# Kernel tuning notes

Measured on AMD Instinct MI355X. Metric: run time of the kernel, lower is better.

Reference implementation:

```python
import jax, jax.numpy as jnp
import numpy as np

B, T, D, R, V = 32, 14, 1024, 4, 8192


def setup_inputs() -> dict:
    key = jax.random.key(0)
    k1, k2, k3, k4, k5 = jax.random.split(key, 5)
    input_embs = jax.random.normal(k1, (B, T, D), dtype=jnp.float32)
    label_ids = jax.random.randint(k2, (B, T), 0, V)
    w_alpha = jax.random.normal(k3, (D, R), dtype=jnp.float32)
    w_beta = jax.random.normal(k4, (D, R), dtype=jnp.float32)
    w_vocab = jax.random.normal(k5, (D, V * R * R), dtype=jnp.float32)
    return {"input_embs": input_embs, "label_ids": label_ids,
            "w_alpha": w_alpha, "w_beta": w_beta, "w_vocab": w_vocab}


def _tt_params(x, w_alpha, w_beta, w_vocab):
    b, t, d = x.shape
    r = w_alpha.shape[1]
    v = w_vocab.shape[1] // (r * r)
    xf = x.reshape(-1, d)
    alpha = jax.nn.sigmoid((xf @ w_alpha).reshape(b, t, r).mean(1)) + 0.001   # (B,R)
    beta = jax.nn.sigmoid((xf @ w_beta).reshape(b, t, r).mean(1)) + 0.001     # (B,R)
    core = jax.nn.sigmoid((xf @ w_vocab).reshape(b, t, r, v, r).mean(1)) * 0.01 + 0.001  # (B,R,V,R)
    return alpha, beta, core


def _chain_matmul(init, mats):
    # init: (B,R,R); mats: (n,B,R,R) -> sequential product init @ mats[0] @ ...
    def step(carry, m):
        return jnp.einsum('bik,bkj->bij', carry, m), None
    out, _ = jax.lax.scan(step, init, mats)
    return out


def reference(input_embs, label_ids, w_alpha, w_beta, w_vocab):
    alpha, beta, core = _tt_params(input_embs, w_alpha, w_beta, w_vocab)
    b, t = label_ids.shape
    # ---- _select: gather core slices at label indices, chain-multiply ----
    sel = core[jnp.arange(b)[:, None], :, label_ids, :]   # (B,T,R,R)
    sel = jnp.swapaxes(sel, 0, 1)                         # (T,B,R,R)
    chain = _chain_matmul(sel[0], sel[1:])                # (B,R,R)
    unnorm = jnp.einsum('bi,bij,bj->b', alpha, chain, beta)
    # ---- normalization: marginalized core multiplied T extra times (T+1 factors, as in source) ----
    cm = core.sum(axis=2)                                 # (B,R,R)
    cm_rep = jnp.broadcast_to(cm, (t,) + cm.shape)        # (T,B,R,R)
    nres = _chain_matmul(cm, cm_rep)                      # (B,R,R)
    norm = jnp.einsum('bi,bij,bj->b', alpha, nres, beta)
    probs = unnorm / norm + 0.001
    loss = -jnp.log(probs)
    return loss.mean()
```

## Files before the change

kernel.cpp:

```cpp
#include <hip/hip_runtime.h>
#include <cstdint>
#include <cstddef>

#define BB 32
#define TT 14
#define DD 1024
#define RR 4
#define VV 8192
#define NCOL (VV*RR*RR)

typedef float f32x16 __attribute__((ext_vector_type(16)));
typedef float f4 __attribute__((ext_vector_type(4)));
typedef short short8 __attribute__((ext_vector_type(8)));
typedef unsigned int uint;


__device__ __forceinline__ uint pack2(float a, float b) {
    return __builtin_amdgcn_perm(__builtin_bit_cast(uint, b),
                                 __builtin_bit_cast(uint, a), 0x07060302u);
}

__device__ __forceinline__ short8 packw(const float* w) {
    uint4 u = make_uint4(pack2(w[0], w[1]), pack2(w[2], w[3]),
                         pack2(w[4], w[5]), pack2(w[6], w[7]));
    return __builtin_bit_cast(short8, u);
}

__global__ __launch_bounds__(256) void k_prep_all(const float* __restrict__ in,
                                                  const float* __restrict__ wa,
                                                  const float* __restrict__ wb,
                                                  ushort* __restrict__ xfrag_us,
                                                  float* __restrict__ alpha,
                                                  float* __restrict__ beta,
                                                  float* __restrict__ cm) {
    __shared__ float xl[DD];
    const int b   = blockIdx.x;
    const int tid = threadIdx.x;
    const int d0  = tid * 4;

    f4 s4 = (f4){0.f, 0.f, 0.f, 0.f};
    #pragma unroll
    for (int t = 0; t < TT; ++t) {
        f4 v = *reinterpret_cast<const f4*>(&in[((b * TT + t) << 10) + d0]);
        s4 += v;
    }
    s4 *= (1.0f / TT);
    *reinterpret_cast<f4*>(&xl[d0]) = s4;

    if (b == 0) { cm[tid] = 0.f; cm[tid + 256] = 0.f; }

    {
        const int s  = d0 >> 4;
        const int h  = (d0 >> 3) & 1;
        const int j0 = d0 & 7;
        uint2 u;
        u.x = pack2(s4.x, s4.y);
        u.y = pack2(s4.z, s4.w);
        *reinterpret_cast<uint2*>(&xfrag_us[((s * 64 + b + 32 * h) << 3) + j0]) = u;
    }

    __syncthreads();

    const int wave = tid >> 6, lane = tid & 63;
    for (int p = wave; p < 8; p += 4) {
        const int r = p >> 1, sf = p & 1;
        const float* wm = sf ? wb : wa;
        float acc = 0.f;
        #pragma unroll
        for (int k = 0; k < 16; ++k) {
            int d = lane + 64 * k;
            acc += xl[d] * wm[d * RR + r];
        }
        #pragma unroll
        for (int m = 1; m < 64; m <<= 1) acc += __shfl_xor(acc, m);
        if (lane == 0) {
            float v = 1.0f / (1.0f + __expf(-acc)) + 0.001f;
            (sf ? beta : alpha)[b * RR + r] = v;
        }
    }
}

#define LOADW(DST, STEP)                                                      \
    _Pragma("unroll")                                                         \
    for (int j = 0; j < 8; ++j)                                               \
        DST[j] = __builtin_nontemporal_load(                                  \
            wp + (size_t)((STEP) * 16 + j) * NCOL);

#define MFMA_STEP(AX, WBUF)                                                   \
    acc = __builtin_amdgcn_mfma_f32_32x32x16_bf16(                            \
        __builtin_bit_cast(short8, AX), packw(WBUF), acc, 0, 0, 0);

__global__ __launch_bounds__(256, 4) void k_core(const float* __restrict__ wv,
                                                 const uint4* __restrict__ xfrag,
                                                 const int*   __restrict__ lab,
                                                 float* __restrict__ cm,
                                                 float* __restrict__ sel) {
    const int tid  = threadIdx.x;
    const int lane = tid & 63;
    const int wvid = tid >> 6;
    const int n0   = blockIdx.x * 128 + wvid * 32;
    const int n    = n0 + (lane & 31);
    const int ii   = n >> 15;
    const int jj   = n & 3;
    const int vv   = (n >> 2) & (VV - 1);

    __shared__ int   lds_lab[BB * TT];
    __shared__ float cm_blk[BB][4];

    const float* wp = wv + (size_t)((lane >> 5) * 8) * NCOL + n;

    f32x16 acc;
    #pragma unroll
    for (int q = 0; q < 16; ++q) acc[q] = 0.f;

    float w0[8], w1[8], w2[8], w3[8];
    uint4 ax0, ax1, ax2, ax3;
    LOADW(w0, 0); ax0 = xfrag[lane];
    LOADW(w1, 1); ax1 = xfrag[64 + lane];
    LOADW(w2, 2); ax2 = xfrag[128 + lane];
    LOADW(w3, 3); ax3 = xfrag[192 + lane];

    #pragma unroll 1
    for (int s = 0; s < 60; s += 4) {
        MFMA_STEP(ax0, w0); LOADW(w0, s + 4); ax0 = xfrag[((s + 4) << 6) + lane];
        MFMA_STEP(ax1, w1); LOADW(w1, s + 5); ax1 = xfrag[((s + 5) << 6) + lane];
        MFMA_STEP(ax2, w2); LOADW(w2, s + 6); ax2 = xfrag[((s + 6) << 6) + lane];
        MFMA_STEP(ax3, w3); LOADW(w3, s + 7); ax3 = xfrag[((s + 7) << 6) + lane];
    }
    MFMA_STEP(ax0, w0);
    MFMA_STEP(ax1, w1);
    MFMA_STEP(ax2, w2);
    MFMA_STEP(ax3, w3);

    for (int idx = tid; idx < BB * TT; idx += 256) lds_lab[idx] = lab[idx];
    if (tid < BB * 4) ((float*)cm_blk)[tid] = 0.f;
    __syncthreads();

    #pragma unroll
    for (int r = 0; r < 16; ++r) {
        float c = 0.01f / (1.0f + __expf(-acc[r])) + 0.001f;
        const int b = (r & 3) + 8 * (r >> 2) + 4 * (lane >> 5);
        float sred = c;
        sred += __shfl_xor(sred, 4);
        sred += __shfl_xor(sred, 8);
        sred += __shfl_xor(sred, 16);
        if ((lane & 31) < 4) atomicAdd(&cm_blk[b][lane & 3], sred);
        #pragma unroll
        for (int t = 0; t < TT; ++t)
            if (lds_lab[b * TT + t] == vv)
                sel[(b * TT + t) * 16 + (ii << 2) + jj] = c;
    }
    __syncthreads();
    if (tid < BB * 4) {
        int b = tid >> 2, j = tid & 3;
        atomicAdd(&cm[b * 16 + (ii << 2) + j], ((float*)cm_blk)[tid]);
    }
}

__global__ __launch_bounds__(64) void k_final(const float* __restrict__ cm,
                                              const float* __restrict__ sel,
                                              const float* __restrict__ alpha,
                                              const float* __restrict__ beta,
                                              float* __restrict__ out) {
    __shared__ float ls[BB];
    int b = threadIdx.x;
    if (b < BB) {
        float ch[16], tmp[16];
        #pragma unroll
        for (int q = 0; q < 16; ++q) ch[q] = sel[(b * TT + 0) * 16 + q];
        for (int t = 1; t < TT; ++t) {
            const float* m = &sel[(b * TT + t) * 16];
            #pragma unroll
            for (int i2 = 0; i2 < 4; ++i2)
                #pragma unroll
                for (int j2 = 0; j2 < 4; ++j2) {
                    float s = 0.f;
                    #pragma unroll
                    for (int k = 0; k < 4; ++k) s += ch[i2*4+k] * m[k*4+j2];
                    tmp[i2*4+j2] = s;
                }
            #pragma unroll
            for (int q = 0; q < 16; ++q) ch[q] = tmp[q];
        }

        float M[16], P[16];
        #pragma unroll
        for (int q = 0; q < 16; ++q) { M[q] = cm[b*16+q]; P[q] = M[q]; }
        for (int t = 0; t < TT; ++t) {
            #pragma unroll
            for (int i2 = 0; i2 < 4; ++i2)
                #pragma unroll
                for (int j2 = 0; j2 < 4; ++j2) {
                    float s = 0.f;
                    #pragma unroll
                    for (int k = 0; k < 4; ++k) s += P[i2*4+k] * M[k*4+j2];
                    tmp[i2*4+j2] = s;
                }
            #pragma unroll
            for (int q = 0; q < 16; ++q) P[q] = tmp[q];
        }

        float a[4], be[4];
        #pragma unroll
        for (int r = 0; r < 4; ++r) { a[r] = alpha[b*4+r]; be[r] = beta[b*4+r]; }
        float un = 0.f, no = 0.f;
        #pragma unroll
        for (int i2 = 0; i2 < 4; ++i2)
            #pragma unroll
            for (int j2 = 0; j2 < 4; ++j2) {
                un += a[i2] * ch[i2*4+j2] * be[j2];
                no += a[i2] * P [i2*4+j2] * be[j2];
            }
        float prob = un / no + 0.001f;
        ls[b] = -logf(prob);
    }
    __syncthreads();
    if (threadIdx.x == 0) {
        float s = 0.f;
        for (int q = 0; q < BB; ++q) s += ls[q];
        out[0] = s / BB;
    }
}

extern "C" void kernel_launch(void* const* d_in, const int* in_sizes, int n_in,
                              void* d_out, int out_size, void* d_ws, size_t ws_size,
                              hipStream_t stream) {
    const float* in_embs = (const float*)d_in[0];
    const int*   lab     = (const int*)  d_in[1];
    const float* wa      = (const float*)d_in[2];
    const float* wb      = (const float*)d_in[3];
    const float* wv      = (const float*)d_in[4];

    float* ws    = (float*)d_ws;
    float* cm    = ws;
    float* sel   = ws + 512;
    float* alpha = ws + 7680;
    float* beta  = ws + 7808;
    uint4* xfrag = (uint4*)(ws + 7936);

    k_prep_all<<<32,   256, 0, stream>>>(in_embs, wa, wb, (ushort*)xfrag,
                                         alpha, beta, cm);
    k_core    <<<1024, 256, 0, stream>>>(wv, xfrag, lab, cm, sel);
    k_final   <<<1,    64,  0, stream>>>(cm, sel, alpha, beta, (float*)d_out);
}
```

Measured before the change: 120.3 us.

## Stage weight tiles into LDS via async global_load_lds with multi-buffer pipeline

The core GEMV-like kernel now copies weight tiles from global memory straight into a four-slot LDS ring using global_load_lds, with explicit vmcnt waits and barriers. Each wave then reads its 8-row fragments from LDS and issues two MFMAs per stage. The block grows to 512 threads covering 512 columns, so the grid shrinks from 1024 to 256 blocks. The goal is fully coalesced, deeper-in-flight loads of the 2 GB/s-bound weight stream, traded against barrier overhead, 128KB of LDS per block, and lower block count and occupancy.

```diff
diff --git a/kernel.cpp b/kernel.cpp
--- a/kernel.cpp
+++ b/kernel.cpp
@@ -8,6 +8,8 @@
 #define RR 4
 #define VV 8192
 #define NCOL (VV*RR*RR)
+#define COLS 512
+#define NTHR 512
 
 typedef float f32x16 __attribute__((ext_vector_type(16)));
 typedef float f4 __attribute__((ext_vector_type(4)));
@@ -80,81 +82,117 @@
     }
 }
 
-#define LOADW(DST, STEP)                                                      \
-    _Pragma("unroll")                                                         \
-    for (int j = 0; j < 8; ++j)                                               \
-        DST[j] = __builtin_nontemporal_load(                                  \
-            wp + (size_t)((STEP) * 16 + j) * NCOL);
-
-#define MFMA_STEP(AX, WBUF)                                                   \
-    acc = __builtin_amdgcn_mfma_f32_32x32x16_bf16(                            \
-        __builtin_bit_cast(short8, AX), packw(WBUF), acc, 0, 0, 0);
-
-__global__ __launch_bounds__(256, 4) void k_core(const float* __restrict__ wv,
+#define STAGE(SG, AXREG)                                                      \
+    do {                                                                      \
+        const int bi_ = (SG) & 3;                                             \
+        _Pragma("unroll")                                                     \
+        for (int r_ = 0; r_ < 4; ++r_) {                                      \
+            const float* gp_ = wv + (size_t)(16 * (SG) + 4 * r_ + srow) * NCOL\
+                               + n0 + scol;                                   \
+            __builtin_amdgcn_global_load_lds(                                 \
+                (const __attribute__((address_space(1))) void*)gp_,           \
+                (__attribute__((address_space(3))) void*)                     \
+                    &buf[bi_][4 * r_ + srow][scol],                           \
+                16, 0, 0);                                                    \
+        }                                                                     \
+        AXREG = xf[((SG) << 6) + lane];                                       \
+    } while (0)
+
+#define COMPUTE(SG, AXREG)                                                    \
+    do {                                                                      \
+        const int bi_ = (SG) & 3;                                             \
+        _Pragma("unroll")                                                     \
+        for (int tau_ = 0; tau_ < 2; ++tau_) {                                \
+            float wr_[8];                                                     \
+            _Pragma("unroll")                                                 \
+            for (int j_ = 0; j_ < 8; ++j_)                                    \
+                wr_[j_] = buf[bi_][rbase + j_][cloc + tau_ * 32];             \
+            acc[tau_] = __builtin_amdgcn_mfma_f32_32x32x16_bf16(              \
+                __builtin_bit_cast(short8, AXREG), packw(wr_), acc[tau_],     \
+                0, 0, 0);                                                     \
+        }                                                                     \
+    } while (0)
+
+#define VMWAIT(N) asm volatile("s_waitcnt vmcnt(" #N ")" ::: "memory")
+#define BAR()     __builtin_amdgcn_s_barrier()
+
+__global__ __launch_bounds__(512, 2) void k_core(const float* __restrict__ wv,
                                                  const uint4* __restrict__ xfrag,
                                                  const int*   __restrict__ lab,
                                                  float* __restrict__ cm,
                                                  float* __restrict__ sel) {
     const int tid  = threadIdx.x;
     const int lane = tid & 63;
-    const int wvid = tid >> 6;
-    const int n0   = blockIdx.x * 128 + wvid * 32;
-    const int n    = n0 + (lane & 31);
-    const int ii   = n >> 15;
-    const int jj   = n & 3;
-    const int vv   = (n >> 2) & (VV - 1);
-
-    __shared__ int   lds_lab[BB * TT];
-    __shared__ float cm_blk[BB][4];
-
-    const float* wp = wv + (size_t)((lane >> 5) * 8) * NCOL + n;
-
-    f32x16 acc;
+    const int w    = tid >> 6;
+    const int n0   = blockIdx.x * COLS;
+    const int ii   = n0 >> 15;
+
+    __shared__ __align__(16) char smem[4 * 16 * COLS * 4];
+    auto buf = reinterpret_cast<float(*)[16][COLS]>(smem);
+
+    const int srow = tid >> 7;
+    const int scol = (tid & 127) << 2;
+    const uint4* xf = xfrag;
+
+    const int rbase = (lane >> 5) * 8;
+    const int cloc  = w * 64 + (lane & 31);
+
+    f32x16 acc[2];
     #pragma unroll
-    for (int q = 0; q < 16; ++q) acc[q] = 0.f;
-
-    float w0[8], w1[8], w2[8], w3[8];
+    for (int t = 0; t < 2; ++t)
+        #pragma unroll
+        for (int q = 0; q < 16; ++q) acc[t][q] = 0.f;
+
     uint4 ax0, ax1, ax2, ax3;
-    LOADW(w0, 0); ax0 = xfrag[lane];
-    LOADW(w1, 1); ax1 = xfrag[64 + lane];
-    LOADW(w2, 2); ax2 = xfrag[128 + lane];
-    LOADW(w3, 3); ax3 = xfrag[192 + lane];
+    STAGE(0, ax0);
+    STAGE(1, ax1);
 
     #pragma unroll 1
-    for (int s = 0; s < 60; s += 4) {
-        MFMA_STEP(ax0, w0); LOADW(w0, s + 4); ax0 = xfrag[((s + 4) << 6) + lane];
-        MFMA_STEP(ax1, w1); LOADW(w1, s + 5); ax1 = xfrag[((s + 5) << 6) + lane];
-        MFMA_STEP(ax2, w2); LOADW(w2, s + 6); ax2 = xfrag[((s + 6) << 6) + lane];
-        MFMA_STEP(ax3, w3); LOADW(w3, s + 7); ax3 = xfrag[((s + 7) << 6) + lane];
-    }
-    MFMA_STEP(ax0, w0);
-    MFMA_STEP(ax1, w1);
-    MFMA_STEP(ax2, w2);
-    MFMA_STEP(ax3, w3);
-
-    for (int idx = tid; idx < BB * TT; idx += 256) lds_lab[idx] = lab[idx];
-    if (tid < BB * 4) ((float*)cm_blk)[tid] = 0.f;
+    for (int s = 0; s < 56; s += 4) {
+        STAGE(s + 2, ax2); VMWAIT(10); BAR(); COMPUTE(s,     ax0);
+        STAGE(s + 3, ax3); VMWAIT(10); BAR(); COMPUTE(s + 1, ax1);
+        STAGE(s + 4, ax0); VMWAIT(10); BAR(); COMPUTE(s + 2, ax2);
+        STAGE(s + 5, ax1); VMWAIT(10); BAR(); COMPUTE(s + 3, ax3);
+    }
+    STAGE(58, ax2); VMWAIT(10); BAR(); COMPUTE(56, ax0);
+    STAGE(59, ax3); VMWAIT(10); BAR(); COMPUTE(57, ax1);
+    STAGE(60, ax0); VMWAIT(10); BAR(); COMPUTE(58, ax2);
+    STAGE(61, ax1); VMWAIT(10); BAR(); COMPUTE(59, ax3);
+    STAGE(62, ax2); VMWAIT(10); BAR(); COMPUTE(60, ax0);
+    STAGE(63, ax3); VMWAIT(10); BAR(); COMPUTE(61, ax1);
+    VMWAIT(5);  BAR(); COMPUTE(62, ax2);
+    VMWAIT(0);  BAR(); COMPUTE(63, ax3);
+
+    __syncthreads();
+    int*   lds_lab = reinterpret_cast<int*>(smem);
+    float* cm_blk  = reinterpret_cast<float*>(smem) + BB * TT;
+    for (int idx = tid; idx < BB * TT; idx += NTHR) lds_lab[idx] = lab[idx];
+    if (tid < BB * 4) cm_blk[tid] = 0.f;
     __syncthreads();
 
     #pragma unroll
-    for (int r = 0; r < 16; ++r) {
-        float c = 0.01f / (1.0f + __expf(-acc[r])) + 0.001f;
-        const int b = (r & 3) + 8 * (r >> 2) + 4 * (lane >> 5);
-        float sred = c;
-        sred += __shfl_xor(sred, 4);
-        sred += __shfl_xor(sred, 8);
-        sred += __shfl_xor(sred, 16);
-        if ((lane & 31) < 4) atomicAdd(&cm_blk[b][lane & 3], sred);
-        #pragma unroll
-        for (int t = 0; t < TT; ++t)
-            if (lds_lab[b * TT + t] == vv)
-                sel[(b * TT + t) * 16 + (ii << 2) + jj] = c;
-    }
-    __syncthreads();
-    if (tid < BB * 4) {
-        int b = tid >> 2, j = tid & 3;
-        atomicAdd(&cm[b * 16 + (ii << 2) + j], ((float*)cm_blk)[tid]);
-    }
+    for (int tau = 0; tau < 2; ++tau) {
+        const int n  = n0 + w * 64 + tau * 32 + (lane & 31);
+        const int jj = n & 3;
+        const int vv = (n >> 2) & (VV - 1);
+        #pragma unroll
+        for (int r = 0; r < 16; ++r) {
+            float c = 0.01f / (1.0f + __expf(-acc[tau][r])) + 0.001f;
+            const int b = (r & 3) + 8 * (r >> 2) + 4 * (lane >> 5);
+            float sred = c;
+            sred += __shfl_xor(sred, 4);
+            sred += __shfl_xor(sred, 8);
+            sred += __shfl_xor(sred, 16);
+            if ((lane & 31) < 4) atomicAdd(&cm_blk[b * 4 + (lane & 3)], sred);
+            #pragma unroll
+            for (int t = 0; t < TT; ++t)
+                if (lds_lab[b * TT + t] == vv)
+                    sel[(b * TT + t) * 16 + (ii << 2) + jj] = c;
+        }
+    }
+    __syncthreads();
+    if (tid < BB * 4)
+        atomicAdd(&cm[(tid >> 2) * 16 + (ii << 2) + (tid & 3)], cm_blk[tid]);
 }
 
 __global__ __launch_bounds__(64) void k_final(const float* __restrict__ cm,
@@ -238,8 +276,8 @@
     float* beta  = ws + 7808;
     uint4* xfrag = (uint4*)(ws + 7936);
 
-    k_prep_all<<<32,   256, 0, stream>>>(in_embs, wa, wb, (ushort*)xfrag,
-                                         alpha, beta, cm);
-    k_core    <<<1024, 256, 0, stream>>>(wv, xfrag, lab, cm, sel);
-    k_final   <<<1,    64,  0, stream>>>(cm, sel, alpha, beta, (float*)d_out);
-}
+    k_prep_all<<<32,  256, 0, stream>>>(in_embs, wa, wb, (ushort*)xfrag,
+                                        alpha, beta, cm);
+    k_core    <<<256, NTHR, 0, stream>>>(wv, xfrag, lab, cm, sel);
+    k_final   <<<1,   64,  0, stream>>>(cm, sel, alpha, beta, (float*)d_out);
+}
```

Measured after the change: 164.7 us. 36.9% more time.
